# Kernel optimization log

Measured on AMD Instinct MI355X. Metric: run time of the kernel, lower is better.

Reference implementation:

```python
import jax, jax.numpy as jnp
import numpy as np

B, T, DIN, DOUT, G = 8, 4096, 1024, 1024, 16
S = T // G  # equal-length contiguous segments


def setup_inputs() -> dict:
    key = jax.random.key(0)
    k1, k2, k3 = jax.random.split(key, 3)
    x = jax.random.normal(k1, (B, T, DIN), dtype=jnp.float32)
    # Embedding(num_groups, dim_in*dim_out) viewed as (dim_out, dim_in) per group
    W = jax.random.normal(k2, (G, DOUT, DIN), dtype=jnp.float32) * (1.0 / np.sqrt(DIN))
    b = jax.random.normal(k3, (G, DOUT), dtype=jnp.float32) * 0.02
    # sorted, contiguous, equal-length segments: [0,...,0,1,...,1,...,G-1]
    indices = jnp.repeat(jnp.arange(G, dtype=jnp.int64), S)
    return {"x": x, "W": W, "b": b, "indices": indices, "num_groups": G}


def reference(x, W, b, indices, num_groups):
    # SegmentLinear: for each contiguous segment of `indices`, apply the
    # group's linear layer out[:, sl] = x[:, sl] @ W[g].T + b[g].
    # With equal-length contiguous segments this is one grouped GEMM.
    Bc, Tc, Din = x.shape
    g = num_groups
    s = Tc // g
    xg = x.reshape(Bc, g, s, Din)                      # [B, G, S, din]
    out = jnp.einsum('bgsd,god->bgso', xg, W)          # grouped GEMM
    out = out + b[None, :, None, :]                    # per-group bias
    return out.reshape(Bc, Tc, -1)
```

## Files before the change

kernel.cpp:

```cpp
#include <hip/hip_runtime.h>

#define B_    8
#define T_    4096
#define DIN_  1024
#define DOUT_ 1024
#define G_    16
#define S_    256

#define BM 256
#define BN 256
#define BK 64
#define NKT (DIN_ / BK)
#define HALF_E 8192

#define NX (B_ * T_ * DIN_)
#define NW (G_ * DOUT_ * DIN_)
#define WS_NEEDED ((size_t)(NX + NW) * 2)

typedef __bf16 bf16x8 __attribute__((ext_vector_type(8)));
typedef float  f32x4  __attribute__((ext_vector_type(4)));

__device__ __forceinline__ void gload_lds16(const void* g, void* l) {
    __builtin_amdgcn_global_load_lds(
        (const __attribute__((address_space(1))) unsigned int*)g,
        (__attribute__((address_space(3))) unsigned int*)l,
        16 , 0, 0);
}

__global__ __launch_bounds__(256)
void cvt_f32_bf16_2(const float* __restrict__ inX, __bf16* __restrict__ outX, int nx8,
                    const float* __restrict__ inW, __bf16* __restrict__ outW, int nw8) {
    const int total = nx8 + nw8;
    int i = blockIdx.x * 256 + threadIdx.x;
    const int stride = gridDim.x * 256;
    for (; i < total; i += stride) {
        const float* in;
        __bf16* out;
        long k;
        if (i < nx8) { in = inX; out = outX; k = (long)i * 8; }
        else         { in = inW; out = outW; k = (long)(i - nx8) * 8; }
        const f32x4 a = *(const f32x4*)(in + k);
        const f32x4 b = *(const f32x4*)(in + k + 4);
        bf16x8 h;
        #pragma unroll
        for (int u = 0; u < 4; ++u) { h[u] = (__bf16)a[u]; h[u + 4] = (__bf16)b[u]; }
        *(bf16x8*)(out + k) = h;
    }
}

__global__ __launch_bounds__(512, 2)
void seg_gemm_bf16(const __bf16* __restrict__ Xb, const __bf16* __restrict__ Wb,
                   const float* __restrict__ Bias, float* __restrict__ Out)
{
    __shared__ __attribute__((aligned(16))) __bf16 As[4 * HALF_E];
    __shared__ __attribute__((aligned(16))) __bf16 Bs[4 * HALF_E];

    const int raw = blockIdx.x;
    const int bid = ((raw & 7) << 6) | (raw >> 3);
    const int g   = bid >> 5;
    const int mT  = (bid >> 2) & 7;
    const int nT  = bid & 3;

    const int tid  = threadIdx.x;
    const int lane = tid & 63;
    const int w    = tid >> 6;
    const int wm   = w >> 2;
    const int wn   = w & 3;

    const long rowBase = (long)mT * T_ + (long)g * S_;
    const long colBase = (long)g * DOUT_ + (long)nT * BN;

    const int srow = w * 16 + (lane >> 2);
    const int scol = ((lane & 3) ^ ((lane >> 3) & 3)) * 8;
    const __bf16* gA = Xb + (rowBase + srow) * DIN_ + scol;
    const __bf16* gB = Wb + (colBase + srow) * DIN_ + scol;
    const int dOff = w * 512 + lane * 8;

    const int ml  = lane & 15;
    const int h   = lane >> 4;
    const int hx8 = (h ^ ((ml >> 1) & 3)) * 8;

    f32x4 acc[8][4] = {};

#define HA(T, KH) (As + ((((T) & 1) << 1) + (KH)) * HALF_E)
#define HB(T, KH) (Bs + ((((T) & 1) << 1) + (KH)) * HALF_E)
#define STG_A(T, KH) do {                                                  \
    const __bf16* p_ = gA + (T) * BK + (KH) * 32;                          \
    gload_lds16(p_,              HA(T, KH) + dOff);                        \
    gload_lds16(p_ + 128 * DIN_, HA(T, KH) + dOff + 4096);                 \
} while (0)
#define STG_B(T, KH) do {                                                  \
    const __bf16* p_ = gB + (T) * BK + (KH) * 32;                          \
    gload_lds16(p_,              HB(T, KH) + dOff);                        \
    gload_lds16(p_ + 128 * DIN_, HB(T, KH) + dOff + 4096);                 \
} while (0)

#define VMW(N)  asm volatile("s_waitcnt vmcnt(" #N ")" ::: "memory")
#define NOPV    ((void)0)

#define PH(T, KH, ILO, NEWB, STAGE, VM, ENDBAR) do {                       \
    const __bf16* Ah_ = HA(T, KH);                                         \
    if (NEWB) {                                                            \
        const __bf16* Bh_ = HB(T, KH);                                     \
        _Pragma("unroll")                                                  \
        for (int j_ = 0; j_ < 4; ++j_)                                     \
            bF[j_] = *(const bf16x8*)&Bh_[(wn * 64 + j_ * 16 + ml) * 32 + hx8]; \
    }                                                                      \
    _Pragma("unroll")                                                      \
    for (int i_ = 0; i_ < 4; ++i_)                                         \
        aF[i_] = *(const bf16x8*)&Ah_[(wm * 128 + ((ILO) + i_) * 16 + ml) * 32 + hx8]; \
    STAGE;                                                                 \
    asm volatile("" ::: "memory");                                         \
    __builtin_amdgcn_s_barrier();                                          \
    __builtin_amdgcn_s_setprio(1);                                         \
    _Pragma("unroll")                                                      \
    for (int i_ = 0; i_ < 4; ++i_)                                         \
        _Pragma("unroll")                                                  \
        for (int j_ = 0; j_ < 4; ++j_)                                     \
            acc[(ILO) + i_][j_] = __builtin_amdgcn_mfma_f32_16x16x32_bf16( \
                aF[i_], bF[j_], acc[(ILO) + i_][j_], 0, 0, 0);             \
    __builtin_amdgcn_s_setprio(0);                                         \
    VM;                                                                    \
    if (ENDBAR) {                                                          \
        asm volatile("" ::: "memory");                                     \
        __builtin_amdgcn_s_barrier();                                      \
        asm volatile("" ::: "memory");                                     \
    }                                                                      \
} while (0)

#define TILE(T, DS01, DS23, VM, LAST) do {                                 \
    bf16x8 aF[4], bF[4];                                                   \
    PH(T, 0, 0, true,  if (DS01) STG_A((T) + 1, 1), NOPV, true);           \
    PH(T, 0, 4, false, if (DS01) STG_B((T) + 1, 1), NOPV, true);           \
    PH(T, 1, 0, true,  if (DS23) STG_A((T) + 2, 0), NOPV, true);           \
    PH(T, 1, 4, false, if (DS23) STG_B((T) + 2, 0), VM, !(LAST));          \
} while (0)

    STG_A(0, 0); STG_B(0, 0); STG_A(0, 1); STG_B(0, 1);
    STG_A(1, 0); STG_B(1, 0);
    VMW(4);
    __builtin_amdgcn_s_barrier();
    asm volatile("" ::: "memory");

    for (int T = 0; T < 14; T += 2) {
        TILE(T,     true, true, VMW(4), false);
        TILE(T + 1, true, true, VMW(4), false);
    }
    TILE(14, true,  false, VMW(0), false);
    TILE(15, false, false, NOPV,   true);

    const int ncolBase = nT * BN + wn * 64;
    #pragma unroll
    for (int j = 0; j < 4; ++j) {
        const int n = ncolBase + j * 16 + ml;
        const float bj = Bias[g * DOUT_ + n];
        #pragma unroll
        for (int i = 0; i < 8; ++i) {
            const long row0 = rowBase + wm * 128 + i * 16 + h * 4;
            #pragma unroll
            for (int r = 0; r < 4; ++r)
                Out[(row0 + r) * DOUT_ + n] = acc[i][j][r] + bj;
        }
    }
#undef TILE
#undef PH
#undef STG_A
#undef STG_B
#undef HA
#undef HB
}

#define FBM 128
#define FBN 128
#define LDKF 40
__global__ __launch_bounds__(256, 2)
void seg_linear_fused(const float* __restrict__ X, const float* __restrict__ W,
                      const float* __restrict__ Bias, float* __restrict__ Out)
{
    __shared__ __attribute__((aligned(16))) __bf16 Asf[FBM * LDKF];
    __shared__ __attribute__((aligned(16))) __bf16 Bsf[FBN * LDKF];

    const int bid = blockIdx.x;
    const int g   = bid >> 7;
    const int rb  = bid & 127;
    const int mT  = rb >> 3;
    const int nT  = rb & 7;

    const int tid  = threadIdx.x;
    const int lane = tid & 63;
    const int wid  = tid >> 6;
    const int wr   = wid >> 1;
    const int wc   = wid & 1;

    const long rowBase = (long)(mT >> 1) * T_ + (long)g * S_ + (mT & 1) * FBM;

    const float* Abase = X + rowBase * DIN_;
    const float* Bbase = W + ((long)g * DOUT_ + (long)nT * FBN) * DIN_;

    const int srow = tid >> 1;
    const int scol = (tid & 1) * 16;
    const float* pA = Abase + (long)srow * DIN_ + scol;
    const float* pB = Bbase + (long)srow * DIN_ + scol;
    __bf16* wA = &Asf[srow * LDKF + scol];
    __bf16* wB = &Bsf[srow * LDKF + scol];

    f32x4 acc[4][4] = {};
    const int q8 = (lane >> 4) * 8;
    const int ml = lane & 15;

    for (int k0 = 0; k0 < DIN_; k0 += 32) {
        f32x4 va0 = *(const f32x4*)(pA + k0);
        f32x4 va1 = *(const f32x4*)(pA + k0 + 4);
        f32x4 va2 = *(const f32x4*)(pA + k0 + 8);
        f32x4 va3 = *(const f32x4*)(pA + k0 + 12);
        f32x4 vb0 = *(const f32x4*)(pB + k0);
        f32x4 vb1 = *(const f32x4*)(pB + k0 + 4);
        f32x4 vb2 = *(const f32x4*)(pB + k0 + 8);
        f32x4 vb3 = *(const f32x4*)(pB + k0 + 12);

        bf16x8 ha0, ha1, hb0, hb1;
        #pragma unroll
        for (int u = 0; u < 4; ++u) {
            ha0[u] = (__bf16)va0[u]; ha0[u + 4] = (__bf16)va1[u];
            ha1[u] = (__bf16)va2[u]; ha1[u + 4] = (__bf16)va3[u];
            hb0[u] = (__bf16)vb0[u]; hb0[u + 4] = (__bf16)vb1[u];
            hb1[u] = (__bf16)vb2[u]; hb1[u + 4] = (__bf16)vb3[u];
        }
        *(bf16x8*)(wA) = ha0; *(bf16x8*)(wA + 8) = ha1;
        *(bf16x8*)(wB) = hb0; *(bf16x8*)(wB + 8) = hb1;

        __syncthreads();

        bf16x8 aF[4], bF[4];
        #pragma unroll
        for (int i = 0; i < 4; ++i)
            aF[i] = *(const bf16x8*)&Asf[(wr * 64 + i * 16 + ml) * LDKF + q8];
        #pragma unroll
        for (int j = 0; j < 4; ++j)
            bF[j] = *(const bf16x8*)&Bsf[(wc * 64 + j * 16 + ml) * LDKF + q8];
        #pragma unroll
        for (int i = 0; i < 4; ++i)
            #pragma unroll
            for (int j = 0; j < 4; ++j)
                acc[i][j] = __builtin_amdgcn_mfma_f32_16x16x32_bf16(aF[i], bF[j], acc[i][j], 0, 0, 0);
        __syncthreads();
    }

    const int mq = lane >> 4;
    const int ncol = nT * FBN + wc * 64;
    #pragma unroll
    for (int j = 0; j < 4; ++j) {
        const int n = ncol + j * 16 + ml;
        const float bj = Bias[g * DOUT_ + n];
        #pragma unroll
        for (int i = 0; i < 4; ++i) {
            const long row0 = rowBase + wr * 64 + i * 16 + mq * 4;
            #pragma unroll
            for (int r = 0; r < 4; ++r)
                Out[(row0 + r) * DOUT_ + n] = acc[i][j][r] + bj;
        }
    }
}

extern "C" void kernel_launch(void* const* d_in, const int* in_sizes, int n_in,
                              void* d_out, int out_size, void* d_ws, size_t ws_size,
                              hipStream_t stream) {
    const float* X    = (const float*)d_in[0];
    const float* W    = (const float*)d_in[1];
    const float* Bias = (const float*)d_in[2];
    float* Out = (float*)d_out;

    if (ws_size >= WS_NEEDED) {
        __bf16* Xb = (__bf16*)d_ws;
        __bf16* Wb = Xb + NX;
        cvt_f32_bf16_2<<<dim3(2048), dim3(256), 0, stream>>>(X, Xb, NX / 8, W, Wb, NW / 8);
        const int grid = G_ * (B_ * S_ / BM) * (DOUT_ / BN);
        seg_gemm_bf16<<<dim3(grid), dim3(512), 0, stream>>>(Xb, Wb, Bias, Out);
    } else {
        const int grid = G_ * (B_ * S_ / FBM) * (DOUT_ / FBN);
        seg_linear_fused<<<dim3(grid), dim3(256), 0, stream>>>(X, W, Bias, Out);
    }
}
```

Before: 155.2 us.

## Restructure GEMM to 4 waves with 128x128 warp tiles and simple double buffer

The bf16 GEMM kernel drops from 512 to 256 threads per block, with each wave now computing a 128x128 sub-tile (8x8 MFMA accumulators) instead of 128x64. This raises register-level reuse of the LDS fragments. The fine-grained four-phase pipeline with interleaved staging and barriers is replaced by a plain double-buffered loop that loads the whole next k-tile, then waits on vmcnt(0) and a barrier each iteration. The conversion kernel is split into two launches with fixed iteration counts, removing the per-element branch. The changes risk heavy register pressure (256 accumulator floats per thread), fewer waves to hide latency, and less overlap between loads and MFMA work.

```diff
diff --git a/kernel.cpp b/kernel.cpp
--- a/kernel.cpp
+++ b/kernel.cpp
@@ -28,17 +28,11 @@
 }
 
 __global__ __launch_bounds__(256)
-void cvt_f32_bf16_2(const float* __restrict__ inX, __bf16* __restrict__ outX, int nx8,
-                    const float* __restrict__ inW, __bf16* __restrict__ outW, int nw8) {
-    const int total = nx8 + nw8;
-    int i = blockIdx.x * 256 + threadIdx.x;
-    const int stride = gridDim.x * 256;
-    for (; i < total; i += stride) {
-        const float* in;
-        __bf16* out;
-        long k;
-        if (i < nx8) { in = inX; out = outX; k = (long)i * 8; }
-        else         { in = inW; out = outW; k = (long)(i - nx8) * 8; }
+void cvt_f32_bf16_fix(const float* __restrict__ in, __bf16* __restrict__ out,
+                      int iters) {
+    const int gid = blockIdx.x * 256 + threadIdx.x;
+    for (int r = 0; r < iters; ++r) {
+        const long k = ((long)r * 524288 + gid) * 8;
         const f32x4 a = *(const f32x4*)(in + k);
         const f32x4 b = *(const f32x4*)(in + k + 4);
         bf16x8 h;
@@ -48,12 +42,12 @@
     }
 }
 
-__global__ __launch_bounds__(512, 2)
+__global__ __launch_bounds__(256, 1)
 void seg_gemm_bf16(const __bf16* __restrict__ Xb, const __bf16* __restrict__ Wb,
                    const float* __restrict__ Bias, float* __restrict__ Out)
 {
-    __shared__ __attribute__((aligned(16))) __bf16 As[4 * HALF_E];
-    __shared__ __attribute__((aligned(16))) __bf16 Bs[4 * HALF_E];
+    __shared__ __attribute__((aligned(16))) __bf16 As[2 * 2 * HALF_E];
+    __shared__ __attribute__((aligned(16))) __bf16 Bs[2 * 2 * HALF_E];
 
     const int raw = blockIdx.x;
     const int bid = ((raw & 7) << 6) | (raw >> 3);
@@ -64,8 +58,8 @@
     const int tid  = threadIdx.x;
     const int lane = tid & 63;
     const int w    = tid >> 6;
-    const int wm   = w >> 2;
-    const int wn   = w & 3;
+    const int wm   = w >> 1;
+    const int wn   = w & 1;
 
     const long rowBase = (long)mT * T_ + (long)g * S_;
     const long colBase = (long)g * DOUT_ + (long)nT * BN;
@@ -80,78 +74,59 @@
     const int h   = lane >> 4;
     const int hx8 = (h ^ ((ml >> 1) & 3)) * 8;
 
-    f32x4 acc[8][4] = {};
-
-#define HA(T, KH) (As + ((((T) & 1) << 1) + (KH)) * HALF_E)
-#define HB(T, KH) (Bs + ((((T) & 1) << 1) + (KH)) * HALF_E)
-#define STG_A(T, KH) do {                                                  \
-    const __bf16* p_ = gA + (T) * BK + (KH) * 32;                          \
-    gload_lds16(p_,              HA(T, KH) + dOff);                        \
-    gload_lds16(p_ + 128 * DIN_, HA(T, KH) + dOff + 4096);                 \
-} while (0)
-#define STG_B(T, KH) do {                                                  \
-    const __bf16* p_ = gB + (T) * BK + (KH) * 32;                          \
-    gload_lds16(p_,              HB(T, KH) + dOff);                        \
-    gload_lds16(p_ + 128 * DIN_, HB(T, KH) + dOff + 4096);                 \
-} while (0)
+    f32x4 acc[8][8] = {};
 
 #define VMW(N)  asm volatile("s_waitcnt vmcnt(" #N ")" ::: "memory")
-#define NOPV    ((void)0)
-
-#define PH(T, KH, ILO, NEWB, STAGE, VM, ENDBAR) do {                       \
-    const __bf16* Ah_ = HA(T, KH);                                         \
-    if (NEWB) {                                                            \
-        const __bf16* Bh_ = HB(T, KH);                                     \
-        _Pragma("unroll")                                                  \
-        for (int j_ = 0; j_ < 4; ++j_)                                     \
-            bF[j_] = *(const bf16x8*)&Bh_[(wn * 64 + j_ * 16 + ml) * 32 + hx8]; \
-    }                                                                      \
-    _Pragma("unroll")                                                      \
-    for (int i_ = 0; i_ < 4; ++i_)                                         \
-        aF[i_] = *(const bf16x8*)&Ah_[(wm * 128 + ((ILO) + i_) * 16 + ml) * 32 + hx8]; \
-    STAGE;                                                                 \
-    asm volatile("" ::: "memory");                                         \
-    __builtin_amdgcn_s_barrier();                                          \
-    __builtin_amdgcn_s_setprio(1);                                         \
-    _Pragma("unroll")                                                      \
-    for (int i_ = 0; i_ < 4; ++i_)                                         \
-        _Pragma("unroll")                                                  \
-        for (int j_ = 0; j_ < 4; ++j_)                                     \
-            acc[(ILO) + i_][j_] = __builtin_amdgcn_mfma_f32_16x16x32_bf16( \
-                aF[i_], bF[j_], acc[(ILO) + i_][j_], 0, 0, 0);             \
-    __builtin_amdgcn_s_setprio(0);                                         \
-    VM;                                                                    \
-    if (ENDBAR) {                                                          \
-        asm volatile("" ::: "memory");                                     \
-        __builtin_amdgcn_s_barrier();                                      \
-        asm volatile("" ::: "memory");                                     \
+
+#define STG(T) do {                                                        \
+    const long ko_ = (long)(T) * BK;                                       \
+    __bf16* a0_ = As + ((T) & 1) * (2 * HALF_E) + dOff;                    \
+    __bf16* b0_ = Bs + ((T) & 1) * (2 * HALF_E) + dOff;                    \
+    _Pragma("unroll")                                                      \
+    for (int r_ = 0; r_ < 4; ++r_) {                                       \
+        const long ro_ = (long)r_ * 64 * DIN_ + ko_;                       \
+        gload_lds16(gA + ro_,      a0_ + r_ * 2048);                       \
+        gload_lds16(gA + ro_ + 32, a0_ + HALF_E + r_ * 2048);              \
+        gload_lds16(gB + ro_,      b0_ + r_ * 2048);                       \
+        gload_lds16(gB + ro_ + 32, b0_ + HALF_E + r_ * 2048);              \
     }                                                                      \
 } while (0)
 
-#define TILE(T, DS01, DS23, VM, LAST) do {                                 \
-    bf16x8 aF[4], bF[4];                                                   \
-    PH(T, 0, 0, true,  if (DS01) STG_A((T) + 1, 1), NOPV, true);           \
-    PH(T, 0, 4, false, if (DS01) STG_B((T) + 1, 1), NOPV, true);           \
-    PH(T, 1, 0, true,  if (DS23) STG_A((T) + 2, 0), NOPV, true);           \
-    PH(T, 1, 4, false, if (DS23) STG_B((T) + 2, 0), VM, !(LAST));          \
+#define KHALF(T, KH) do {                                                  \
+    const __bf16* Ah_ = As + ((T) & 1) * (2 * HALF_E) + (KH) * HALF_E;     \
+    const __bf16* Bh_ = Bs + ((T) & 1) * (2 * HALF_E) + (KH) * HALF_E;     \
+    bf16x8 aF[8], bF[8];                                                   \
+    _Pragma("unroll")                                                      \
+    for (int i_ = 0; i_ < 8; ++i_)                                         \
+        aF[i_] = *(const bf16x8*)&Ah_[(wm * 128 + i_ * 16 + ml) * 32 + hx8]; \
+    _Pragma("unroll")                                                      \
+    for (int j_ = 0; j_ < 8; ++j_)                                         \
+        bF[j_] = *(const bf16x8*)&Bh_[(wn * 128 + j_ * 16 + ml) * 32 + hx8]; \
+    _Pragma("unroll")                                                      \
+    for (int i_ = 0; i_ < 8; ++i_)                                         \
+        _Pragma("unroll")                                                  \
+        for (int j_ = 0; j_ < 8; ++j_)                                     \
+            acc[i_][j_] = __builtin_amdgcn_mfma_f32_16x16x32_bf16(         \
+                aF[i_], bF[j_], acc[i_][j_], 0, 0, 0);                     \
 } while (0)
 
-    STG_A(0, 0); STG_B(0, 0); STG_A(0, 1); STG_B(0, 1);
-    STG_A(1, 0); STG_B(1, 0);
-    VMW(4);
+    STG(0);
+    VMW(0);
     __builtin_amdgcn_s_barrier();
     asm volatile("" ::: "memory");
 
-    for (int T = 0; T < 14; T += 2) {
-        TILE(T,     true, true, VMW(4), false);
-        TILE(T + 1, true, true, VMW(4), false);
-    }
-    TILE(14, true,  false, VMW(0), false);
-    TILE(15, false, false, NOPV,   true);
-
-    const int ncolBase = nT * BN + wn * 64;
+    for (int t = 0; t < NKT; ++t) {
+        if (t + 1 < NKT) STG(t + 1);
+        KHALF(t, 0);
+        KHALF(t, 1);
+        VMW(0);
+        __builtin_amdgcn_s_barrier();
+        asm volatile("" ::: "memory");
+    }
+
+    const int ncolBase = nT * BN + wn * 128;
     #pragma unroll
-    for (int j = 0; j < 4; ++j) {
+    for (int j = 0; j < 8; ++j) {
         const int n = ncolBase + j * 16 + ml;
         const float bj = Bias[g * DOUT_ + n];
         #pragma unroll
@@ -162,12 +137,8 @@
                 Out[(row0 + r) * DOUT_ + n] = acc[i][j][r] + bj;
         }
     }
-#undef TILE
-#undef PH
-#undef STG_A
-#undef STG_B
-#undef HA
-#undef HB
+#undef KHALF
+#undef STG
 }
 
 #define FBM 128
@@ -273,9 +244,10 @@
     if (ws_size >= WS_NEEDED) {
         __bf16* Xb = (__bf16*)d_ws;
         __bf16* Wb = Xb + NX;
-        cvt_f32_bf16_2<<<dim3(2048), dim3(256), 0, stream>>>(X, Xb, NX / 8, W, Wb, NW / 8);
+        cvt_f32_bf16_fix<<<dim3(2048), dim3(256), 0, stream>>>(X, Xb, 8);
+        cvt_f32_bf16_fix<<<dim3(2048), dim3(256), 0, stream>>>(W, Wb, 4);
         const int grid = G_ * (B_ * S_ / BM) * (DOUT_ / BN);
-        seg_gemm_bf16<<<dim3(grid), dim3(512), 0, stream>>>(Xb, Wb, Bias, Out);
+        seg_gemm_bf16<<<dim3(grid), dim3(256), 0, stream>>>(Xb, Wb, Bias, Out);
     } else {
         const int grid = G_ * (B_ * S_ / FBM) * (DOUT_ / FBN);
         seg_linear_fused<<<dim3(grid), dim3(256), 0, stream>>>(X, W, Bias, Out);
```

After: 192.8 us. 1.24x slower.
